# Kernel tuning notes

Measured on AMD Instinct MI355X. Metric: run time of the kernel, lower is better.

The kernel has to match this reference:

```python
import jax, jax.numpy as jnp
import numpy as np

N_NODES = 50000
N_EDGES = 1600000
N_GRAPHS = 64
DIM_IN, DIM_H, HEADS, DIM_OUT = 128, 32, 2, 64
NEG_SLOPE = 0.2


def _segment_softmax(scores, seg, num_segments):
    # scores: [E, H], seg: [E] int -> softmax over edges sharing the same dst
    m = jax.ops.segment_max(scores, seg, num_segments=num_segments)
    m = jnp.where(jnp.isfinite(m), m, 0.0)  # empty segments -> -inf; neutralize
    e = jnp.exp(scores - m[seg])
    s = jax.ops.segment_sum(e, seg, num_segments=num_segments)
    return e / (s[seg] + 1e-16)


def gatv2_conv(x, edge_index, Wl, Wr, att, bias, heads, ch, n_nodes):
    # PyG GATv2Conv defaults: add_self_loops=True, share_weights=False, concat heads.
    loops = jnp.arange(n_nodes, dtype=edge_index.dtype)
    ei = jnp.concatenate([edge_index, jnp.stack([loops, loops])], axis=1)
    src, dst = ei[0], ei[1]
    xl = (x @ Wl).reshape(n_nodes, heads, ch)  # source transform
    xr = (x @ Wr).reshape(n_nodes, heads, ch)  # target transform
    el = xl[src]                               # [E+N, H, C] gather
    s = jax.nn.leaky_relu(el + xr[dst], NEG_SLOPE)
    scores = jnp.einsum('ehc,hc->eh', s, att)  # [E+N, H]
    alpha = _segment_softmax(scores, dst, n_nodes)
    out = jax.ops.segment_sum(alpha[..., None] * el, dst, num_segments=n_nodes)
    return out.reshape(n_nodes, heads * ch) + bias


def setup_inputs() -> dict:
    key = jax.random.key(0)
    ks = jax.random.split(key, 12)
    glorot = lambda k, shp: jax.random.normal(k, shp, jnp.float32) * np.sqrt(2.0 / (shp[0] + shp[-1]))
    x = jax.random.normal(ks[0], (N_NODES, DIM_IN), jnp.float32)
    edge_index = jax.random.randint(ks[1], (2, N_EDGES), 0, N_NODES, jnp.int64)
    batch = jnp.sort(jax.random.randint(ks[2], (N_NODES,), 0, N_GRAPHS, jnp.int64))
    H1 = DIM_H * HEADS
    return {
        'x': x, 'edge_index': edge_index, 'batch': batch,
        'Wl1': glorot(ks[3], (DIM_IN, H1)), 'Wr1': glorot(ks[4], (DIM_IN, H1)),
        'att1': glorot(ks[5], (HEADS, DIM_H)), 'b1': jnp.zeros((H1,), jnp.float32),
        'Wl2': glorot(ks[6], (H1, DIM_OUT)), 'Wr2': glorot(ks[7], (H1, DIM_OUT)),
        'att2': glorot(ks[8], (1, DIM_OUT)), 'b2': jnp.zeros((DIM_OUT,), jnp.float32),
        'lin_w': glorot(ks[9], (DIM_OUT, 2)), 'lin_b': jnp.zeros((2,), jnp.float32),
    }


def reference(x, edge_index, batch, Wl1, Wr1, att1, b1, Wl2, Wr2, att2, b2, lin_w, lin_b):
    # eval mode: dropout is identity
    h = gatv2_conv(x, edge_index, Wl1, Wr1, att1, b1, HEADS, DIM_H, N_NODES)
    h = jax.nn.elu(h)
    h = jax.nn.elu(gatv2_conv(h, edge_index, Wl2, Wr2, att2, b2, 1, DIM_OUT, N_NODES))
    # global mean pool over graphs
    sums = jax.ops.segment_sum(h, batch, num_segments=N_GRAPHS)
    cnts = jax.ops.segment_sum(jnp.ones((N_NODES,), h.dtype), batch, num_segments=N_GRAPHS)
    pooled = sums / jnp.maximum(cnts, 1.0)[:, None]
    return pooled @ lin_w + lin_b
```

## Files before the change

kernel.cpp:

```cpp
#include <hip/hip_runtime.h>
#include <hip/hip_bf16.h>
#include <math.h>

#define N_NODES 50000
#define N_EDGES 1600000
#define N_GRAPHS 64
#define NB 391
#define NBLK 256
#define CHUNK 6250
#define ROW_STRIDE 80

template <int CTRL>
__device__ __forceinline__ float dpp_add(float v) {
    int r = __builtin_amdgcn_update_dpp(0, __builtin_bit_cast(int, v), CTRL, 0xF, 0xF, true);
    return v + __builtin_bit_cast(float, r);
}

__device__ __forceinline__ float red8(float v) {
    v = dpp_add<0xB1>(v);
    v = dpp_add<0x4E>(v);
    v = dpp_add<0x141>(v);
    return v;
}

__device__ __forceinline__ float red16(float v) {
    v = red8(v);
    v = dpp_add<0x140>(v);
    return v;
}

__device__ __forceinline__ float4 lrelu4(float4 u) {
    float4 r;
    r.x = fmaxf(u.x, 0.2f * u.x);
    r.y = fmaxf(u.y, 0.2f * u.y);
    r.z = fmaxf(u.z, 0.2f * u.z);
    r.w = fmaxf(u.w, 0.2f * u.w);
    return r;
}

template <int K>
__global__ __launch_bounds__(256) void gemm_tiled(
    const float* __restrict__ x, const float* __restrict__ Wl,
    const float* __restrict__ Wr, float* __restrict__ xl, float* __restrict__ xr) {
    __shared__ float xs[64][K + 1];
    const int t = threadIdx.x;
    const int base = blockIdx.x * 64;
    const int nf4 = 64 * K / 4;
    for (int f = t; f < nf4; f += 256) {
        const int row = f / (K / 4);
        const int c4 = f % (K / 4);
        float4 v = make_float4(0.f, 0.f, 0.f, 0.f);
        if (base + row < N_NODES)
            v = *(const float4*)(x + (size_t)(base + row) * K + c4 * 4);
        xs[row][c4 * 4 + 0] = v.x;
        xs[row][c4 * 4 + 1] = v.y;
        xs[row][c4 * 4 + 2] = v.z;
        xs[row][c4 * 4 + 3] = v.w;
    }
    __syncthreads();
    const int lane = t & 63;
    const int w = __builtin_amdgcn_readfirstlane(t >> 6);
    const float* __restrict__ W = (w < 2) ? Wl : Wr;
    const int cb = (w & 1) * 32;
    float acc[32];
#pragma unroll
    for (int j = 0; j < 32; ++j) acc[j] = 0.f;
#pragma unroll 2
    for (int k = 0; k < K; ++k) {
        const float xv = xs[lane][k];
        const float* __restrict__ Wrow = W + k * 64 + cb;
#pragma unroll
        for (int j = 0; j < 32; ++j) acc[j] = fmaf(xv, Wrow[j], acc[j]);
    }
    const int n = base + lane;
    if (n < N_NODES) {
        float* __restrict__ o = (w < 2) ? xl : xr;
#pragma unroll
        for (int j = 0; j < 32; j += 4) {
            float4 v = {acc[j], acc[j + 1], acc[j + 2], acc[j + 3]};
            *(float4*)(o + (size_t)n * 64 + cb + j) = v;
        }
    }
}

__global__ __launch_bounds__(256) void count_kernel(
    const int* __restrict__ ei, int* __restrict__ countsRM) {
    __shared__ int h[NB];
    const int t = threadIdx.x;
    for (int k = t; k < NB; k += 256) h[k] = 0;
    __syncthreads();
    const int base = blockIdx.x * CHUNK;
    for (int e = base + t; e < base + CHUNK; e += 256)
        atomicAdd(&h[ei[N_EDGES + e] >> 7], 1);
    __syncthreads();
    for (int k = t; k < NB; k += 256) countsRM[blockIdx.x * NB + k] = h[k];
}

__global__ __launch_bounds__(256) void scan_bucket(
    const int* __restrict__ countsRM, int* __restrict__ scanT,
    int* __restrict__ totals) {
    __shared__ int tmp[256];
    const int b = blockIdx.x;
    const int t = threadIdx.x;
    const int v0 = countsRM[t * NB + b];
    tmp[t] = v0;
    __syncthreads();
    for (int off = 1; off < 256; off <<= 1) {
        int v = (t >= off) ? tmp[t - off] : 0;
        __syncthreads();
        tmp[t] += v;
        __syncthreads();
    }
    scanT[b * 256 + t] = tmp[t] - v0;
    if (t == 255) totals[b] = tmp[t];
}

__global__ __launch_bounds__(512) void scan_total(
    const int* __restrict__ totals, int* __restrict__ bucketBase) {
    __shared__ int tmp[512];
    const int t = threadIdx.x;
    const int v0 = (t < NB) ? totals[t] : 0;
    tmp[t] = v0;
    __syncthreads();
    for (int off = 1; off < 512; off <<= 1) {
        int v = (t >= off) ? tmp[t - off] : 0;
        __syncthreads();
        tmp[t] += v;
        __syncthreads();
    }
    if (t < NB) bucketBase[t] = tmp[t] - v0;
    if (t == NB - 1) bucketBase[NB] = tmp[t];
}

__global__ __launch_bounds__(256) void scatter2_kernel(
    const int* __restrict__ ei, const int* __restrict__ scanT,
    const int* __restrict__ bucketBase, int* __restrict__ sortedE) {
    __shared__ int cursor[NB];
    const int t = threadIdx.x;
    const int b = blockIdx.x;
    for (int k = t; k < NB; k += 256)
        cursor[k] = bucketBase[k] + scanT[k * 256 + b];
    __syncthreads();
    const int base = b * CHUNK;
    for (int e = base + t; e < base + CHUNK; e += 256) {
        const int s = ei[e];
        const int d = ei[N_EDGES + e];
        const int idx = atomicAdd(&cursor[d >> 7], 1);
        sortedE[idx] = (s << 7) | (d & 127);
    }
}

__global__ __launch_bounds__(256) void expand_kernel(
    const int* __restrict__ bucketBase, const int* __restrict__ sortedE,
    int* __restrict__ deg, int* __restrict__ rows) {
    __shared__ int ldeg[128];
    const int b = blockIdx.x;
    const int t = threadIdx.x;
    if (t < 128) ldeg[t] = 0;
    __syncthreads();
    const int beg = bucketBase[b];
    const int end = bucketBase[b + 1];
    const int node_base = b * 128;
    for (int i = beg + t; i < end; i += 256) {
        const int en = sortedE[i];
        const int ld = en & 127;
        const int pos = atomicAdd(&ldeg[ld], 1);
        if (pos < ROW_STRIDE) rows[(node_base + ld) * ROW_STRIDE + pos] = en >> 7;
    }
    __syncthreads();
    if (t < 128) {
        const int n = node_base + t;
        if (n < N_NODES) {
            int c = ldeg[t];
            deg[n] = c < ROW_STRIDE ? c : ROW_STRIDE;
        }
    }
}

template <bool L1HEADS>
__device__ __forceinline__ float edge_ev4(float4 a, float4 xr4, float4 at4, bool valid) {
    float4 u;
    u.x = a.x + xr4.x; u.y = a.y + xr4.y; u.z = a.z + xr4.z; u.w = a.w + xr4.w;
    float4 l = lrelu4(u);
    float v = at4.x * l.x;
    v = fmaf(at4.y, l.y, v);
    v = fmaf(at4.z, l.z, v);
    v = fmaf(at4.w, l.w, v);
    v = L1HEADS ? red8(v) : red16(v);
    float ev = __expf(v);
    return valid ? ev : 0.f;
}

template <bool L1HEADS>
__global__ __launch_bounds__(256) void node_layer(
    const int* __restrict__ deg, const int* __restrict__ rows,
    const float* __restrict__ xl, const float* __restrict__ xr,
    const float* __restrict__ att, const float* __restrict__ bias,
    float* __restrict__ hout) {
    const int n = (blockIdx.x * 256 + threadIdx.x) >> 6;
    const int lane = threadIdx.x & 63;
    const int sub = lane & 15;
    const int g = lane >> 4;
    const float4 xr4 = *(const float4*)(xr + (size_t)n * 64 + sub * 4);
    const float4 xl4 = *(const float4*)(xl + (size_t)n * 64 + sub * 4);
    const float4 at4 = *(const float4*)(att + sub * 4);

    float ev = edge_ev4<L1HEADS>(xl4, xr4, at4, g == 0);
    float4 acc;
    acc.x = ev * xl4.x; acc.y = ev * xl4.y; acc.z = ev * xl4.z; acc.w = ev * xl4.w;
    float ssum = ev;

    const int cnt = __builtin_amdgcn_readfirstlane(deg[n]);
    const int* __restrict__ row = rows + n * ROW_STRIDE;
    for (int i = 0; i < cnt; i += 8) {
        const int e0 = i + g, e1 = i + 4 + g;
        const bool v0 = e0 < cnt, v1 = e1 < cnt;
        const int s0 = v0 ? row[e0] : 0;
        const int s1 = v1 ? row[e1] : 0;
        const float4 a0 = *(const float4*)(xl + (size_t)s0 * 64 + sub * 4);
        const float4 a1 = *(const float4*)(xl + (size_t)s1 * 64 + sub * 4);
        const float ev0 = edge_ev4<L1HEADS>(a0, xr4, at4, v0);
        const float ev1 = edge_ev4<L1HEADS>(a1, xr4, at4, v1);
        acc.x = fmaf(ev0, a0.x, acc.x); acc.x = fmaf(ev1, a1.x, acc.x);
        acc.y = fmaf(ev0, a0.y, acc.y); acc.y = fmaf(ev1, a1.y, acc.y);
        acc.z = fmaf(ev0, a0.z, acc.z); acc.z = fmaf(ev1, a1.z, acc.z);
        acc.w = fmaf(ev0, a0.w, acc.w); acc.w = fmaf(ev1, a1.w, acc.w);
        ssum += ev0 + ev1;
    }
    acc.x += __shfl_xor(acc.x, 16); acc.x += __shfl_xor(acc.x, 32);
    acc.y += __shfl_xor(acc.y, 16); acc.y += __shfl_xor(acc.y, 32);
    acc.z += __shfl_xor(acc.z, 16); acc.z += __shfl_xor(acc.z, 32);
    acc.w += __shfl_xor(acc.w, 16); acc.w += __shfl_xor(acc.w, 32);
    ssum  += __shfl_xor(ssum, 16);  ssum  += __shfl_xor(ssum, 32);
    if (g == 0) {
        const float inv = 1.f / (ssum + 1e-16f);
        const float4 b4 = *(const float4*)(bias + sub * 4);
        float4 o;
        o.x = acc.x * inv + b4.x;
        o.y = acc.y * inv + b4.y;
        o.z = acc.z * inv + b4.z;
        o.w = acc.w * inv + b4.w;
        o.x = o.x > 0.f ? o.x : expm1f(o.x);
        o.y = o.y > 0.f ? o.y : expm1f(o.y);
        o.z = o.z > 0.f ? o.z : expm1f(o.z);
        o.w = o.w > 0.f ? o.w : expm1f(o.w);
        *(float4*)(hout + (size_t)n * 64 + sub * 4) = o;
    }
}

__global__ __launch_bounds__(64) void pool_kernel(
    const float* __restrict__ h2, const int* __restrict__ batch,
    float* __restrict__ pooled, float* __restrict__ cnt) {
    const int t = threadIdx.x;
    const int base = blockIdx.x * 64;
    float local = 0.f, lc = 0.f;
    int cur = -1;
    for (int j = 0; j < 64; ++j) {
        const int n = base + j;
        if (n >= N_NODES) break;
        const int g = batch[n];
        if (g != cur) {
            if (cur >= 0) {
                unsafeAtomicAdd(&pooled[cur * 64 + t], local);
                if (t == 0) unsafeAtomicAdd(&cnt[cur], lc);
            }
            cur = g; local = 0.f; lc = 0.f;
        }
        local += h2[n * 64 + t];
        lc += 1.f;
    }
    if (cur >= 0) {
        unsafeAtomicAdd(&pooled[cur * 64 + t], local);
        if (t == 0) unsafeAtomicAdd(&cnt[cur], lc);
    }
}

__global__ __launch_bounds__(128) void head_kernel(
    const float* __restrict__ pooled, const float* __restrict__ cnt,
    const float* __restrict__ lin_w, const float* __restrict__ lin_b,
    float* __restrict__ out) {
    const int i = threadIdx.x;
    const int g = i >> 1, k = i & 1;
    float c = cnt[g];
    c = c > 1.f ? c : 1.f;
    float a = 0.f;
#pragma unroll
    for (int j = 0; j < 64; ++j) a = fmaf(pooled[g * 64 + j] / c, lin_w[j * 2 + k], a);
    out[i] = a + lin_b[k];
}

extern "C" void kernel_launch(void* const* d_in, const int* in_sizes, int n_in,
                              void* d_out, int out_size, void* d_ws, size_t ws_size,
                              hipStream_t stream) {
    const float* x     = (const float*)d_in[0];
    const int*   ei    = (const int*)d_in[1];
    const int*   batch = (const int*)d_in[2];
    const float* Wl1   = (const float*)d_in[3];
    const float* Wr1   = (const float*)d_in[4];
    const float* att1  = (const float*)d_in[5];
    const float* b1    = (const float*)d_in[6];
    const float* Wl2   = (const float*)d_in[7];
    const float* Wr2   = (const float*)d_in[8];
    const float* att2  = (const float*)d_in[9];
    const float* b2    = (const float*)d_in[10];
    const float* lin_w = (const float*)d_in[11];
    const float* lin_b = (const float*)d_in[12];

    float* ws = (float*)d_ws;
    float* xl       = ws;
    float* xr       = ws + 3200000;
    float* h1       = ws + 6400000;
    int*   rows     = (int*)(ws + 9600000);
    int*   deg      = (int*)(ws + 13603840);
    int*   countsRM = (int*)(ws + 13653888);
    int*   scanT    = (int*)(ws + 13753984);
    int*   totals   = (int*)(ws + 13854080);
    int*   bb       = (int*)(ws + 13854592);
    float* pooled   = ws + 13855104;
    float* cnt      = ws + 13859200;
    int*   sortedE  = (int*)(ws + 13859264);

    hipMemsetAsync(pooled, 0, (size_t)(4096 + 64) * sizeof(float), stream);

    count_kernel<<<NBLK, 256, 0, stream>>>(ei, countsRM);
    scan_bucket<<<NB, 256, 0, stream>>>(countsRM, scanT, totals);
    scan_total<<<1, 512, 0, stream>>>(totals, bb);
    scatter2_kernel<<<NBLK, 256, 0, stream>>>(ei, scanT, bb, sortedE);
    expand_kernel<<<NB, 256, 0, stream>>>(bb, sortedE, deg, rows);

    const int gblocks = (N_NODES + 63) / 64;

    gemm_tiled<128><<<gblocks, 256, 0, stream>>>(x, Wl1, Wr1, xl, xr);
    node_layer<true><<<N_NODES / 4, 256, 0, stream>>>(deg, rows, xl, xr, att1, b1, h1);

    gemm_tiled<64><<<gblocks, 256, 0, stream>>>(h1, Wl2, Wr2, xl, xr);
    node_layer<false><<<N_NODES / 4, 256, 0, stream>>>(deg, rows, xl, xr, att2, b2, h1);

    pool_kernel<<<(N_NODES + 63) / 64, 64, 0, stream>>>(h1, batch, pooled, cnt);
    head_kernel<<<1, 128, 0, stream>>>(pooled, cnt, lin_w, lin_b, (float*)d_out);
}
```

Measured before the change: 331.0 us.

## Store source features as bf16 and fuse edge counting into first GEMM

The source-side transform xl is now written as packed bf16 and unpacked in the node aggregation kernels. This halves the bytes of the random per-edge gather, which dominates the aggregation. The edge-count histogram kernel is merged into the layer-1 GEMM launch as extra blocks, so counting runs alongside the GEMM and one launch is removed. The cost is reduced precision in attention scores and aggregated messages, and some extra branching in the GEMM kernel.

```diff
diff --git a/kernel.cpp b/kernel.cpp
--- a/kernel.cpp
+++ b/kernel.cpp
@@ -10,6 +10,8 @@
 #define CHUNK 6250
 #define ROW_STRIDE 80
 
+typedef unsigned int u32;
+
 template <int CTRL>
 __device__ __forceinline__ float dpp_add(float v) {
     int r = __builtin_amdgcn_update_dpp(0, __builtin_bit_cast(int, v), CTRL, 0xF, 0xF, true);
@@ -38,12 +40,40 @@
     return r;
 }
 
-template <int K>
+__device__ __forceinline__ float4 unpack_bf16x4(uint2 u) {
+    float4 a;
+    a.x = __builtin_bit_cast(float, u.x << 16);
+    a.y = __builtin_bit_cast(float, u.x & 0xFFFF0000u);
+    a.z = __builtin_bit_cast(float, u.y << 16);
+    a.w = __builtin_bit_cast(float, u.y & 0xFFFF0000u);
+    return a;
+}
+
+__device__ __forceinline__ u32 pack_bf16x2(float lo, float hi) {
+    unsigned short l = __builtin_bit_cast(unsigned short, __float2bfloat16(lo));
+    unsigned short h = __builtin_bit_cast(unsigned short, __float2bfloat16(hi));
+    return (u32)l | ((u32)h << 16);
+}
+
+template <int K, bool FUSE_COUNT>
 __global__ __launch_bounds__(256) void gemm_tiled(
     const float* __restrict__ x, const float* __restrict__ Wl,
-    const float* __restrict__ Wr, float* __restrict__ xl, float* __restrict__ xr) {
+    const float* __restrict__ Wr, u32* __restrict__ xlb, float* __restrict__ xr,
+    const int* __restrict__ ei, int* __restrict__ countsRM, int gemmBlocks) {
     __shared__ float xs[64][K + 1];
     const int t = threadIdx.x;
+    if (FUSE_COUNT && blockIdx.x >= gemmBlocks) {
+        int* h = (int*)&xs[0][0];
+        const int cb = blockIdx.x - gemmBlocks;
+        for (int k = t; k < NB; k += 256) h[k] = 0;
+        __syncthreads();
+        const int base = cb * CHUNK;
+        for (int e = base + t; e < base + CHUNK; e += 256)
+            atomicAdd(&h[ei[N_EDGES + e] >> 7], 1);
+        __syncthreads();
+        for (int k = t; k < NB; k += 256) countsRM[cb * NB + k] = h[k];
+        return;
+    }
     const int base = blockIdx.x * 64;
     const int nf4 = 64 * K / 4;
     for (int f = t; f < nf4; f += 256) {
@@ -74,26 +104,22 @@
     }
     const int n = base + lane;
     if (n < N_NODES) {
-        float* __restrict__ o = (w < 2) ? xl : xr;
-#pragma unroll
-        for (int j = 0; j < 32; j += 4) {
-            float4 v = {acc[j], acc[j + 1], acc[j + 2], acc[j + 3]};
-            *(float4*)(o + (size_t)n * 64 + cb + j) = v;
+        if (w < 2) {
+            u32 pk[16];
+#pragma unroll
+            for (int j = 0; j < 32; j += 2) pk[j >> 1] = pack_bf16x2(acc[j], acc[j + 1]);
+            uint4* dst = (uint4*)(xlb + (size_t)n * 32 + (w & 1) * 16);
+#pragma unroll
+            for (int j = 0; j < 4; ++j)
+                dst[j] = make_uint4(pk[j * 4], pk[j * 4 + 1], pk[j * 4 + 2], pk[j * 4 + 3]);
+        } else {
+#pragma unroll
+            for (int j = 0; j < 32; j += 4) {
+                float4 v = {acc[j], acc[j + 1], acc[j + 2], acc[j + 3]};
+                *(float4*)(xr + (size_t)n * 64 + cb + j) = v;
+            }
         }
     }
-}
-
-__global__ __launch_bounds__(256) void count_kernel(
-    const int* __restrict__ ei, int* __restrict__ countsRM) {
-    __shared__ int h[NB];
-    const int t = threadIdx.x;
-    for (int k = t; k < NB; k += 256) h[k] = 0;
-    __syncthreads();
-    const int base = blockIdx.x * CHUNK;
-    for (int e = base + t; e < base + CHUNK; e += 256)
-        atomicAdd(&h[ei[N_EDGES + e] >> 7], 1);
-    __syncthreads();
-    for (int k = t; k < NB; k += 256) countsRM[blockIdx.x * NB + k] = h[k];
 }
 
 __global__ __launch_bounds__(256) void scan_bucket(
@@ -194,7 +220,7 @@
 template <bool L1HEADS>
 __global__ __launch_bounds__(256) void node_layer(
     const int* __restrict__ deg, const int* __restrict__ rows,
-    const float* __restrict__ xl, const float* __restrict__ xr,
+    const u32* __restrict__ xlb, const float* __restrict__ xr,
     const float* __restrict__ att, const float* __restrict__ bias,
     float* __restrict__ hout) {
     const int n = (blockIdx.x * 256 + threadIdx.x) >> 6;
@@ -202,7 +228,7 @@
     const int sub = lane & 15;
     const int g = lane >> 4;
     const float4 xr4 = *(const float4*)(xr + (size_t)n * 64 + sub * 4);
-    const float4 xl4 = *(const float4*)(xl + (size_t)n * 64 + sub * 4);
+    const float4 xl4 = unpack_bf16x4(*(const uint2*)(xlb + (size_t)n * 32 + sub * 2));
     const float4 at4 = *(const float4*)(att + sub * 4);
 
     float ev = edge_ev4<L1HEADS>(xl4, xr4, at4, g == 0);
@@ -217,8 +243,8 @@
         const bool v0 = e0 < cnt, v1 = e1 < cnt;
         const int s0 = v0 ? row[e0] : 0;
         const int s1 = v1 ? row[e1] : 0;
-        const float4 a0 = *(const float4*)(xl + (size_t)s0 * 64 + sub * 4);
-        const float4 a1 = *(const float4*)(xl + (size_t)s1 * 64 + sub * 4);
+        const float4 a0 = unpack_bf16x4(*(const uint2*)(xlb + (size_t)s0 * 32 + sub * 2));
+        const float4 a1 = unpack_bf16x4(*(const uint2*)(xlb + (size_t)s1 * 32 + sub * 2));
         const float ev0 = edge_ev4<L1HEADS>(a0, xr4, at4, v0);
         const float ev1 = edge_ev4<L1HEADS>(a1, xr4, at4, v1);
         acc.x = fmaf(ev0, a0.x, acc.x); acc.x = fmaf(ev1, a1.x, acc.x);
@@ -307,34 +333,36 @@
     const float* lin_b = (const float*)d_in[12];
 
     float* ws = (float*)d_ws;
-    float* xl       = ws;
-    float* xr       = ws + 3200000;
-    float* h1       = ws + 6400000;
-    int*   rows     = (int*)(ws + 9600000);
-    int*   deg      = (int*)(ws + 13603840);
-    int*   countsRM = (int*)(ws + 13653888);
-    int*   scanT    = (int*)(ws + 13753984);
-    int*   totals   = (int*)(ws + 13854080);
-    int*   bb       = (int*)(ws + 13854592);
-    float* pooled   = ws + 13855104;
-    float* cnt      = ws + 13859200;
-    int*   sortedE  = (int*)(ws + 13859264);
+    u32*   xlb      = (u32*)ws;
+    float* xr       = ws + 1600000;
+    float* h1       = ws + 4800000;
+    int*   rows     = (int*)(ws + 8000000);
+    int*   deg      = (int*)(ws + 12003840);
+    int*   countsRM = (int*)(ws + 12053888);
+    int*   scanT    = (int*)(ws + 12153984);
+    int*   totals   = (int*)(ws + 12254080);
+    int*   bb       = (int*)(ws + 12254592);
+    float* pooled   = ws + 12255104;
+    float* cnt      = ws + 12259200;
+    int*   sortedE  = (int*)(ws + 12259264);
 
     hipMemsetAsync(pooled, 0, (size_t)(4096 + 64) * sizeof(float), stream);
 
-    count_kernel<<<NBLK, 256, 0, stream>>>(ei, countsRM);
+    const int gblocks = (N_NODES + 63) / 64;
+
+    gemm_tiled<128, true><<<gblocks + NBLK, 256, 0, stream>>>(
+        x, Wl1, Wr1, xlb, xr, ei, countsRM, gblocks);
+
     scan_bucket<<<NB, 256, 0, stream>>>(countsRM, scanT, totals);
     scan_total<<<1, 512, 0, stream>>>(totals, bb);
     scatter2_kernel<<<NBLK, 256, 0, stream>>>(ei, scanT, bb, sortedE);
     expand_kernel<<<NB, 256, 0, stream>>>(bb, sortedE, deg, rows);
 
-    const int gblocks = (N_NODES + 63) / 64;
-
-    gemm_tiled<128><<<gblocks, 256, 0, stream>>>(x, Wl1, Wr1, xl, xr);
-    node_layer<true><<<N_NODES / 4, 256, 0, stream>>>(deg, rows, xl, xr, att1, b1, h1);
-
-    gemm_tiled<64><<<gblocks, 256, 0, stream>>>(h1, Wl2, Wr2, xl, xr);
-    node_layer<false><<<N_NODES / 4, 256, 0, stream>>>(deg, rows, xl, xr, att2, b2, h1);
+    node_layer<true><<<N_NODES / 4, 256, 0, stream>>>(deg, rows, xlb, xr, att1, b1, h1);
+
+    gemm_tiled<64, false><<<gblocks, 256, 0, stream>>>(
+        h1, Wl2, Wr2, xlb, xr, nullptr, nullptr, gblocks);
+    node_layer<false><<<N_NODES / 4, 256, 0, stream>>>(deg, rows, xlb, xr, att2, b2, h1);
 
     pool_kernel<<<(N_NODES + 63) / 64, 64, 0, stream>>>(h1, batch, pooled, cnt);
     head_kernel<<<1, 128, 0, stream>>>(pooled, cnt, lin_w, lin_b, (float*)d_out);
```

Result: faster. 318.9 us (-3.7%).
